# Kernel optimization log

Measured on AMD Instinct MI355X. Metric: run time of the kernel, lower is better.

The kernel has to match this reference:

```python
import jax, jax.numpy as jnp
import numpy as np

B, N, C_IN, H, C_OUT = 8, 1024, 256, 4, 256
C = C_OUT // H  # per-head dim = 64
ALPHA = 0.2
NEG_INF = -9e15


def setup_inputs() -> dict:
    key = jax.random.key(0)
    k1, k2, k3, k4, k5 = jax.random.split(key, 5)
    node_feats = jax.random.normal(k1, (B, N, C_IN), dtype=jnp.float32)
    adj_matrix = jax.random.randint(k2, (B, N, N), 0, 2, dtype=jnp.int32)
    # include self-loops as GAT expects
    eye = jnp.eye(N, dtype=jnp.int32)[None]
    adj_matrix = jnp.maximum(adj_matrix, eye)
    # xavier_uniform with gain=1.414
    def xavier(k, shape, fan_in, fan_out, gain=1.414):
        lim = gain * np.sqrt(6.0 / (fan_in + fan_out))
        return jax.random.uniform(k, shape, jnp.float32, -lim, lim)
    W = xavier(k3, (C_OUT, C_IN), C_IN, C_OUT)          # projection weight [out,in]
    b = jnp.zeros((C_OUT,), dtype=jnp.float32)           # projection bias
    a = xavier(k4, (H, 2 * C), 2 * C, H)                 # attention vector per head
    return {"node_feats": node_feats, "adj_matrix": adj_matrix, "W": W, "b": b, "a": a}


def reference(node_feats, adj_matrix, W, b, a):
    Bb, Nn, _ = node_feats.shape
    Hh, twoC = a.shape
    Cc = twoC // 2
    # linear projection -> [B, N, H, C]
    h = (node_feats @ W.T + b).reshape(Bb, Nn, Hh, Cc)
    # edge logit(i,j) = leakyrelu(a . [h_i, h_j]) = leakyrelu(a1.h_i + a2.h_j)
    a_src, a_dst = a[:, :Cc], a[:, Cc:]
    l_src = jnp.einsum('bihc,hc->bih', h, a_src)  # [B,N,H]
    l_dst = jnp.einsum('bjhc,hc->bjh', h, a_dst)  # [B,N,H]
    logits = jax.nn.leaky_relu(l_src[:, :, None, :] + l_dst[:, None, :, :], ALPHA)  # [B,N,N,H]
    logits = jnp.where(adj_matrix[..., None] == 1, logits, NEG_INF)
    probs = jax.nn.softmax(logits, axis=2)  # softmax over neighbors j
    out = jnp.einsum('bijh,bjhc->bihc', probs, h)  # aggregate
    return out.reshape(Bb, Nn, Hh * Cc)  # concat heads
```

## Files before the change

kernel.cpp:

```cpp
#include <hip/hip_runtime.h>
#include <hip/hip_bf16.h>

#define BN   8
#define NN   1024
#define CIN  256
#define COUT 256
#define HH   4
#define CC   64
#define ALPHA_C 0.2f

typedef __attribute__((ext_vector_type(8))) short short8;
typedef __attribute__((ext_vector_type(4))) float f32x4;

__device__ __forceinline__ unsigned short f2bf(float x) {
    __hip_bfloat16 h = __float2bfloat16(x);
    return *(unsigned short*)&h;
}
__device__ __forceinline__ float bf2f(unsigned short u) {
    return __uint_as_float(((unsigned int)u) << 16);
}
__device__ __forceinline__ void gl_lds16(const void* g, void* l) {
    __builtin_amdgcn_global_load_lds(
        (const __attribute__((address_space(1))) void*)g,
        (__attribute__((address_space(3))) void*)l, 16, 0, 0);
}

__global__ __launch_bounds__(256) void kprep(
    const float* __restrict__ W, const int* __restrict__ adj,
    unsigned short* __restrict__ Whp, unsigned short* __restrict__ Wlp,
    unsigned int* __restrict__ bmG)
{
    if (blockIdx.x < 2048) {
        const int bid = blockIdx.x;
        const int b  = bid & 7;
        const int rl = bid >> 3;
        const int wv = threadIdx.x >> 6;
        const int l  = threadIdx.x & 63;
        const int row = b * NN + rl * 4 + wv;
        const int* arow = adj + (size_t)row * NN;
        #pragma unroll 4
        for (int it = 0; it < 16; ++it) {
            int av = arow[it * 64 + l];
            unsigned long long mb = __ballot(av != 0);
            if (l == 0) {
                bmG[row * 32 + 2 * it    ] = (unsigned int)mb;
                bmG[row * 32 + 2 * it + 1] = (unsigned int)(mb >> 32);
            }
        }
    } else {
        const int bid = blockIdx.x - 2048;
        const int n = threadIdx.x;
        const int fi = n * 64 + (bid >> 2) * 8 + (bid & 3) * 2;
        const float4* W4 = (const float4*)W;
        float4 wa = W4[fi], wb = W4[fi + 1];
        float xs[8] = {wa.x, wa.y, wa.z, wa.w, wb.x, wb.y, wb.z, wb.w};
        unsigned short hh[8], ll[8];
        #pragma unroll
        for (int e = 0; e < 8; ++e) {
            hh[e] = f2bf(xs[e]);
            ll[e] = f2bf(xs[e] - bf2f(hh[e]));
        }
        *(uint4*)(Whp + ((size_t)bid * 256 + n) * 8) = *(uint4*)hh;
        *(uint4*)(Wlp + ((size_t)bid * 256 + n) * 8) = *(uint4*)ll;
    }
}

__global__ __launch_bounds__(1024, 1) void k1_gemm(
    const float* __restrict__ X, const float* __restrict__ bias, const float* __restrict__ a,
    const unsigned short* __restrict__ Whp, const unsigned short* __restrict__ Wlp,
    unsigned short* __restrict__ hbf_p, float* __restrict__ lsrc_t, float* __restrict__ ldst_t)
{
    __shared__ __align__(16) unsigned short Xh[32 * 256];
    __shared__ __align__(16) unsigned short Xl[32 * 256];
    __shared__ float lsP[2][8][2][16];

    const int bid = blockIdx.x;
    const int b  = bid & 7;
    const int tj = bid >> 3;
    const int row0 = b * NN + tj * 32;
    const int tid = threadIdx.x;
    const int wv = tid >> 6, l = tid & 63, il = l & 15, jg = l >> 4;
    const int mq = wv >> 3, no = wv & 7;

    {
        const float4* X4 = (const float4*)(X + (size_t)row0 * CIN);
        #pragma unroll
        for (int it = 0; it < 2; ++it) {
            int f = it * 1024 + tid;
            int r = f >> 6, k4 = f & 63;
            float4 x = X4[f];
            unsigned short h0 = f2bf(x.x), h1 = f2bf(x.y), h2 = f2bf(x.z), h3 = f2bf(x.w);
            unsigned short l0 = f2bf(x.x - bf2f(h0)), l1 = f2bf(x.y - bf2f(h1));
            unsigned short l2 = f2bf(x.z - bf2f(h2)), l3 = f2bf(x.w - bf2f(h3));
            unsigned short hs[4] = {h0, h1, h2, h3}, ls[4] = {l0, l1, l2, l3};
            int off = r * 512 + ((k4 * 8) ^ ((r & 7) << 4));
            *(uint2*)((char*)Xh + off) = *(uint2*)hs;
            *(uint2*)((char*)Xl + off) = *(uint2*)ls;
        }
    }
    __syncthreads();

    f32x4 acc0 = {0.f, 0.f, 0.f, 0.f}, acc1 = acc0;
    {
        const int abase = (mq * 16 + il) * 512;
        const int swz = (il & 7) << 4;
        const short8* Wh8 = (const short8*)Whp;
        const short8* Wl8 = (const short8*)Wlp;
        const int nb = no * 32 + il;
        #pragma unroll
        for (int kc = 0; kc < 8; ++kc) {
            const int ab = abase + ((kc * 64 + jg * 16) ^ swz);
            short8 Ah = *(const short8*)((const char*)Xh + ab);
            short8 Al = *(const short8*)((const char*)Xl + ab);
            const int pidx = (kc * 4 + jg) * 256 + nb;
            short8 Bh0 = Wh8[pidx],      Bl0 = Wl8[pidx];
            short8 Bh1 = Wh8[pidx + 16], Bl1 = Wl8[pidx + 16];
            acc0 = __builtin_amdgcn_mfma_f32_16x16x32_bf16(Ah, Bh0, acc0, 0, 0, 0);
            acc1 = __builtin_amdgcn_mfma_f32_16x16x32_bf16(Ah, Bh1, acc1, 0, 0, 0);
            acc0 = __builtin_amdgcn_mfma_f32_16x16x32_bf16(Ah, Bl0, acc0, 0, 0, 0);
            acc1 = __builtin_amdgcn_mfma_f32_16x16x32_bf16(Ah, Bl1, acc1, 0, 0, 0);
            acc0 = __builtin_amdgcn_mfma_f32_16x16x32_bf16(Al, Bh0, acc0, 0, 0, 0);
            acc1 = __builtin_amdgcn_mfma_f32_16x16x32_bf16(Al, Bh1, acc1, 0, 0, 0);
        }
    }

    const int c0 = no * 32 + il, c1 = c0 + 16;
    const float bia0 = bias[c0], bia1 = bias[c1];
    const int hh = no >> 1;
    const int cc0 = c0 & 63, cc1 = c1 & 63;
    const float as0 = a[hh * 128 + cc0],      as1 = a[hh * 128 + cc1];
    const float ad0 = a[hh * 128 + 64 + cc0], ad1 = a[hh * 128 + 64 + cc1];

    float v0[4], v1[4], psrc[4], pdst[4];
    #pragma unroll
    for (int r = 0; r < 4; ++r) {
        v0[r] = acc0[r] + bia0;
        v1[r] = acc1[r] + bia1;
        psrc[r] = v0[r] * as0 + v1[r] * as1;
        pdst[r] = v0[r] * ad0 + v1[r] * ad1;
    }
    #pragma unroll
    for (int off = 8; off >= 1; off >>= 1) {
        #pragma unroll
        for (int r = 0; r < 4; ++r) {
            psrc[r] += __shfl_xor(psrc[r], off);
            pdst[r] += __shfl_xor(pdst[r], off);
        }
    }
    __syncthreads();

    unsigned short* hp = Xh;
    #pragma unroll
    for (int r = 0; r < 4; ++r) {
        int m = mq * 16 + 4 * jg + r;
        int base = (m >> 3) * 128 + (m & 7);
        hp[(c0 >> 6) * 2048 + ((c0 & 63) >> 4) * 512 + base + (c0 & 15) * 8] = f2bf(v0[r]);
        hp[(c1 >> 6) * 2048 + ((c1 & 63) >> 4) * 512 + base + (c1 & 15) * 8] = f2bf(v1[r]);
    }
    if (il == 0) {
        #pragma unroll
        for (int r = 0; r < 4; ++r) {
            lsP[0][no][mq][4 * jg + r] = psrc[r];
            lsP[1][no][mq][4 * jg + r] = pdst[r];
        }
    }
    __syncthreads();

    {
        uint4* dst4 = (uint4*)(hbf_p + (size_t)(b * 32 + tj) * 8192);
        dst4[tid] = ((const uint4*)hp)[tid];
    }
    if (tid < 256) {
        int sd = tid >> 7, rem = tid & 127, h2 = rem >> 5, m = rem & 31;
        float v = lsP[sd][2 * h2][m >> 4][m & 15] + lsP[sd][2 * h2 + 1][m >> 4][m & 15];
        float* dst = sd ? ldst_t : lsrc_t;
        dst[((size_t)b * HH + h2) * NN + tj * 32 + m] = v;
    }
}

__global__ __launch_bounds__(1024, 1) void k2_attn(
    const unsigned short* __restrict__ hbf_p, const unsigned int* __restrict__ bmG,
    const float* __restrict__ lsrc_t, const float* __restrict__ ldst_t,
    float* __restrict__ out)
{
    __shared__ __align__(16) char smem[151808];
    __shared__ float lsumS[4][4][32];

    unsigned short* hS  = (unsigned short*)smem;
    unsigned int*  bmS  = (unsigned int*)(smem + 131072);
    float*        ldstS = (float*)(smem + 147712);

    const int bid = blockIdx.x;
    const int b  = bid & 7;
    const int h  = (bid >> 3) & 3;
    const int i0 = (bid >> 5) * 128;
    const int tid = threadIdx.x;
    const int wv = tid >> 6, l = tid & 63, il = l & 15, jg = l >> 4;
    const int rg = wv >> 2, jq = wv & 3;

    {
        #pragma unroll
        for (int k = 0; k < 2; ++k) {
            const int tj = wv * 2 + k;
            #pragma unroll
            for (int cs = 0; cs < 4; ++cs) {
                gl_lds16(hbf_p + ((((size_t)(b * 32 + tj)) * 1024 + h * 256 + cs * 64 + l) << 3),
                         hS + (size_t)(tj * 256 + cs * 64 + l) * 8);
            }
        }
    }
    {
        const unsigned int* bsrc = bmG + ((size_t)(b * NN + i0)) * 32;
        #pragma unroll
        for (int k = 0; k < 4; ++k) {
            int idx = k * 1024 + tid;
            int r = idx >> 5, w = idx & 31;
            bmS[w * 130 + r] = bsrc[idx];
        }
    }
    if (tid < 256)
        ((float4*)ldstS)[tid] = ((const float4*)(ldst_t + ((size_t)(b * HH + h)) * NN))[tid];

    const float* lsrc_b = lsrc_t + ((size_t)(b * HH + h)) * NN + i0 + rg * 32;
    const float lsv0 = lsrc_b[il];
    const float lsv1 = lsrc_b[16 + il];

    __syncthreads();

    float mx = -3.4e38f;
    #pragma unroll
    for (int jt = 0; jt < 16; ++jt) mx = fmaxf(mx, ldstS[jt * 64 + l]);
    #pragma unroll
    for (int off = 32; off >= 1; off >>= 1) mx = fmaxf(mx, __shfl_xor(mx, off));
    float mr0, mr1;
    { float t_ = lsv0 + mx; mr0 = fmaxf(t_, ALPHA_C * t_); }
    { float t_ = lsv1 + mx; mr1 = fmaxf(t_, ALPHA_C * t_); }
    float ls0 = 0.f, ls1 = 0.f;

    f32x4 z4 = {0.f,0.f,0.f,0.f};
    f32x4 a00 = z4, a01 = z4, a02 = z4, a03 = z4;
    f32x4 a10 = z4, a11 = z4, a12 = z4, a13 = z4;

    const short8* hS8 = (const short8*)hS;

    #pragma unroll 2
    for (int t = 0; t < 8; ++t) {
        const int tj = jq * 8 + t;
        short8 c0 = hS8[tj * 256 +   0 + l];
        short8 c1 = hS8[tj * 256 +  64 + l];
        short8 c2 = hS8[tj * 256 + 128 + l];
        short8 c3 = hS8[tj * 256 + 192 + l];
        const unsigned int bw0 = bmS[tj * 130 + rg * 32 + il] >> (jg * 8);
        const unsigned int bw1 = bmS[tj * 130 + rg * 32 + 16 + il] >> (jg * 8);
        const float4 dA = *(const float4*)(ldstS + tj * 32 + jg * 8);
        const float4 dB = *(const float4*)(ldstS + tj * 32 + jg * 8 + 4);

        short8 af0, af1;
        #define PELEM(AF, E, DV, BWV, LSV, MR, LS) {             \
            float s_ = (LSV) + (DV);                             \
            s_ = fmaxf(s_, ALPHA_C * s_);                        \
            float p_ = __expf(s_ - (MR));                        \
            p_ = ((BWV >> (E)) & 1u) ? p_ : 0.f;                 \
            LS += p_;                                            \
            AF[E] = (short)(__float_as_uint(p_) >> 16); }
        PELEM(af0, 0, dA.x, bw0, lsv0, mr0, ls0)
        PELEM(af0, 1, dA.y, bw0, lsv0, mr0, ls0)
        PELEM(af0, 2, dA.z, bw0, lsv0, mr0, ls0)
        PELEM(af0, 3, dA.w, bw0, lsv0, mr0, ls0)
        PELEM(af0, 4, dB.x, bw0, lsv0, mr0, ls0)
        PELEM(af0, 5, dB.y, bw0, lsv0, mr0, ls0)
        PELEM(af0, 6, dB.z, bw0, lsv0, mr0, ls0)
        PELEM(af0, 7, dB.w, bw0, lsv0, mr0, ls0)
        PELEM(af1, 0, dA.x, bw1, lsv1, mr1, ls1)
        PELEM(af1, 1, dA.y, bw1, lsv1, mr1, ls1)
        PELEM(af1, 2, dA.z, bw1, lsv1, mr1, ls1)
        PELEM(af1, 3, dA.w, bw1, lsv1, mr1, ls1)
        PELEM(af1, 4, dB.x, bw1, lsv1, mr1, ls1)
        PELEM(af1, 5, dB.y, bw1, lsv1, mr1, ls1)
        PELEM(af1, 6, dB.z, bw1, lsv1, mr1, ls1)
        PELEM(af1, 7, dB.w, bw1, lsv1, mr1, ls1)
        #undef PELEM

        a00 = __builtin_amdgcn_mfma_f32_16x16x32_bf16(af0, c0, a00, 0, 0, 0);
        a01 = __builtin_amdgcn_mfma_f32_16x16x32_bf16(af0, c1, a01, 0, 0, 0);
        a02 = __builtin_amdgcn_mfma_f32_16x16x32_bf16(af0, c2, a02, 0, 0, 0);
        a03 = __builtin_amdgcn_mfma_f32_16x16x32_bf16(af0, c3, a03, 0, 0, 0);
        a10 = __builtin_amdgcn_mfma_f32_16x16x32_bf16(af1, c0, a10, 0, 0, 0);
        a11 = __builtin_amdgcn_mfma_f32_16x16x32_bf16(af1, c1, a11, 0, 0, 0);
        a12 = __builtin_amdgcn_mfma_f32_16x16x32_bf16(af1, c2, a12, 0, 0, 0);
        a13 = __builtin_amdgcn_mfma_f32_16x16x32_bf16(af1, c3, a13, 0, 0, 0);
    }

    ls0 += __shfl_xor(ls0, 16); ls0 += __shfl_xor(ls0, 32);
    ls1 += __shfl_xor(ls1, 16); ls1 += __shfl_xor(ls1, 32);
    if (l < 16) {
        lsumS[jq][rg][il] = ls0;
        lsumS[jq][rg][16 + il] = ls1;
    }
    __syncthreads();

    float* red0 = (float*)smem;
    float* red1 = red0 + 128 * 68;
    {
        float* rb = (jq & 1) ? red1 : red0;
        const int rbase = rg * 32 + 4 * jg;
        #define STROW(ACC, ROFF, CS, OP) {                                   \
            rb[(rbase + (ROFF) + 0) * 68 + (CS) * 16 + il] OP ACC[0];        \
            rb[(rbase + (ROFF) + 1) * 68 + (CS) * 16 + il] OP ACC[1];        \
            rb[(rbase + (ROFF) + 2) * 68 + (CS) * 16 + il] OP ACC[2];        \
            rb[(rbase + (ROFF) + 3) * 68 + (CS) * 16 + il] OP ACC[3]; }
        #define STOREALL(OP) {                                               \
            STROW(a00, 0, 0, OP) STROW(a01, 0, 1, OP)                        \
            STROW(a02, 0, 2, OP) STROW(a03, 0, 3, OP)                        \
            STROW(a10, 16, 0, OP) STROW(a11, 16, 1, OP)                      \
            STROW(a12, 16, 2, OP) STROW(a13, 16, 3, OP) }
        if (jq < 2) STOREALL(=)
        __syncthreads();
        if (jq >= 2) STOREALL(+=)
        __syncthreads();
        #undef STROW
        #undef STOREALL
    }

    #pragma unroll
    for (int pass = 0; pass < 2; ++pass) {
        int row = pass * 64 + (tid >> 4);
        int c4  = tid & 15;
        float4 v0 = *(const float4*)(red0 + row * 68 + c4 * 4);
        float4 v1 = *(const float4*)(red1 + row * 68 + c4 * 4);
        float ls = lsumS[0][row >> 5][row & 31] + lsumS[1][row >> 5][row & 31]
                 + lsumS[2][row >> 5][row & 31] + lsumS[3][row >> 5][row & 31];
        float inv = 1.0f / ls;
        float4 o = make_float4((v0.x + v1.x) * inv, (v0.y + v1.y) * inv,
                               (v0.z + v1.z) * inv, (v0.w + v1.w) * inv);
        *(float4*)(out + ((size_t)(b * NN + i0 + row)) * COUT + h * 64 + c4 * 4) = o;
    }
}

extern "C" void kernel_launch(void* const* d_in, const int* in_sizes, int n_in,
                              void* d_out, int out_size, void* d_ws, size_t ws_size,
                              hipStream_t stream) {
    const float* X    = (const float*)d_in[0];
    const int*   adj  = (const int*)  d_in[1];
    const float* W    = (const float*)d_in[2];
    const float* bias = (const float*)d_in[3];
    const float* a    = (const float*)d_in[4];
    float* out = (float*)d_out;

    unsigned short* hbf_p = (unsigned short*)d_ws;
    float* lsrc_t = (float*)(hbf_p + (size_t)BN * 32 * 8192);
    float* ldst_t = lsrc_t + (size_t)BN * HH * NN;
    unsigned short* Whp = (unsigned short*)(ldst_t + (size_t)BN * HH * NN);
    unsigned short* Wlp = Whp + 65536;
    unsigned int*   bmG = (unsigned int*)(Wlp + 65536);

    kprep<<<2048 + 32, 256, 0, stream>>>(W, adj, Whp, Wlp, bmG);
    k1_gemm<<<256, 1024, 0, stream>>>(X, bias, a, Whp, Wlp, hbf_p, lsrc_t, ldst_t);
    k2_attn<<<256, 1024, 0, stream>>>(hbf_p, bmG, lsrc_t, ldst_t, out);
}
```

Before: 41.51 us.

## Fuse adjacency bitmask build into GEMM kernel and streamline softmax exp

```diff
diff --git a/kernel.cpp b/kernel.cpp
--- a/kernel.cpp
+++ b/kernel.cpp
@@ -8,6 +8,13 @@
 #define HH   4
 #define CC   64
 #define ALPHA_C 0.2f
+#define LOG2E_C 1.4426950408889634f
+
+#if __has_builtin(__builtin_amdgcn_exp2f)
+#define EXP2F(x) __builtin_amdgcn_exp2f(x)
+#else
+#define EXP2F(x) exp2f(x)
+#endif
 
 typedef __attribute__((ext_vector_type(8))) short short8;
 typedef __attribute__((ext_vector_type(4))) float f32x4;
@@ -25,50 +32,30 @@
         (__attribute__((address_space(3))) void*)l, 16, 0, 0);
 }
 
-__global__ __launch_bounds__(256) void kprep(
-    const float* __restrict__ W, const int* __restrict__ adj,
-    unsigned short* __restrict__ Whp, unsigned short* __restrict__ Wlp,
-    unsigned int* __restrict__ bmG)
+__global__ __launch_bounds__(256) void kw_pack(
+    const float* __restrict__ W, unsigned short* __restrict__ Whp, unsigned short* __restrict__ Wlp)
 {
-    if (blockIdx.x < 2048) {
-        const int bid = blockIdx.x;
-        const int b  = bid & 7;
-        const int rl = bid >> 3;
-        const int wv = threadIdx.x >> 6;
-        const int l  = threadIdx.x & 63;
-        const int row = b * NN + rl * 4 + wv;
-        const int* arow = adj + (size_t)row * NN;
-        #pragma unroll 4
-        for (int it = 0; it < 16; ++it) {
-            int av = arow[it * 64 + l];
-            unsigned long long mb = __ballot(av != 0);
-            if (l == 0) {
-                bmG[row * 32 + 2 * it    ] = (unsigned int)mb;
-                bmG[row * 32 + 2 * it + 1] = (unsigned int)(mb >> 32);
-            }
-        }
-    } else {
-        const int bid = blockIdx.x - 2048;
-        const int n = threadIdx.x;
-        const int fi = n * 64 + (bid >> 2) * 8 + (bid & 3) * 2;
-        const float4* W4 = (const float4*)W;
-        float4 wa = W4[fi], wb = W4[fi + 1];
-        float xs[8] = {wa.x, wa.y, wa.z, wa.w, wb.x, wb.y, wb.z, wb.w};
-        unsigned short hh[8], ll[8];
-        #pragma unroll
-        for (int e = 0; e < 8; ++e) {
-            hh[e] = f2bf(xs[e]);
-            ll[e] = f2bf(xs[e] - bf2f(hh[e]));
-        }
-        *(uint4*)(Whp + ((size_t)bid * 256 + n) * 8) = *(uint4*)hh;
-        *(uint4*)(Wlp + ((size_t)bid * 256 + n) * 8) = *(uint4*)ll;
-    }
+    const int bid = blockIdx.x;
+    const int n = threadIdx.x;
+    const int fi = n * 64 + (bid >> 2) * 8 + (bid & 3) * 2;
+    const float4* W4 = (const float4*)W;
+    float4 wa = W4[fi], wb = W4[fi + 1];
+    float xs[8] = {wa.x, wa.y, wa.z, wa.w, wb.x, wb.y, wb.z, wb.w};
+    unsigned short hh[8], ll[8];
+    #pragma unroll
+    for (int e = 0; e < 8; ++e) {
+        hh[e] = f2bf(xs[e]);
+        ll[e] = f2bf(xs[e] - bf2f(hh[e]));
+    }
+    *(uint4*)(Whp + ((size_t)bid * 256 + n) * 8) = *(uint4*)hh;
+    *(uint4*)(Wlp + ((size_t)bid * 256 + n) * 8) = *(uint4*)ll;
 }
 
 __global__ __launch_bounds__(1024, 1) void k1_gemm(
     const float* __restrict__ X, const float* __restrict__ bias, const float* __restrict__ a,
-    const unsigned short* __restrict__ Whp, const unsigned short* __restrict__ Wlp,
-    unsigned short* __restrict__ hbf_p, float* __restrict__ lsrc_t, float* __restrict__ ldst_t)
+    const int* __restrict__ adj, const unsigned short* __restrict__ Whp,
+    const unsigned short* __restrict__ Wlp, unsigned short* __restrict__ hbf_p,
+    float* __restrict__ lsrc_t, float* __restrict__ ldst_t, unsigned int* __restrict__ bmG)
 {
     __shared__ __align__(16) unsigned short Xh[32 * 256];
     __shared__ __align__(16) unsigned short Xl[32 * 256];
@@ -81,6 +68,25 @@
     const int tid = threadIdx.x;
     const int wv = tid >> 6, l = tid & 63, il = l & 15, jg = l >> 4;
     const int mq = wv >> 3, no = wv & 7;
+
+    {
+        #pragma unroll
+        for (int rr = 0; rr < 2; ++rr) {
+            const int r = 2 * wv + rr;
+            const int* ap = adj + ((size_t)(row0 + r)) * NN;
+            int av[16];
+            #pragma unroll
+            for (int it = 0; it < 16; ++it) av[it] = ap[it * 64 + l];
+            #pragma unroll
+            for (int it = 0; it < 16; ++it) {
+                unsigned long long mb = __ballot(av[it] != 0);
+                if (l == 0) {
+                    bmG[((size_t)(row0 + r)) * 32 + 2 * it    ] = (unsigned int)mb;
+                    bmG[((size_t)(row0 + r)) * 32 + 2 * it + 1] = (unsigned int)(mb >> 32);
+                }
+            }
+        }
+    }
 
     {
         const float4* X4 = (const float4*)(X + (size_t)row0 * CIN);
@@ -218,12 +224,15 @@
             bmS[w * 130 + r] = bsrc[idx];
         }
     }
-    if (tid < 256)
-        ((float4*)ldstS)[tid] = ((const float4*)(ldst_t + ((size_t)(b * HH + h)) * NN))[tid];
+    if (tid < 256) {
+        float4 v = ((const float4*)(ldst_t + ((size_t)(b * HH + h)) * NN))[tid];
+        v.x *= LOG2E_C; v.y *= LOG2E_C; v.z *= LOG2E_C; v.w *= LOG2E_C;
+        ((float4*)ldstS)[tid] = v;
+    }
 
     const float* lsrc_b = lsrc_t + ((size_t)(b * HH + h)) * NN + i0 + rg * 32;
-    const float lsv0 = lsrc_b[il];
-    const float lsv1 = lsrc_b[16 + il];
+    const float lsv0 = lsrc_b[il] * LOG2E_C;
+    const float lsv1 = lsrc_b[16 + il] * LOG2E_C;
 
     __syncthreads();
 
@@ -235,15 +244,16 @@
     float mr0, mr1;
     { float t_ = lsv0 + mx; mr0 = fmaxf(t_, ALPHA_C * t_); }
     { float t_ = lsv1 + mx; mr1 = fmaxf(t_, ALPHA_C * t_); }
-    float ls0 = 0.f, ls1 = 0.f;
 
     f32x4 z4 = {0.f,0.f,0.f,0.f};
     f32x4 a00 = z4, a01 = z4, a02 = z4, a03 = z4;
     f32x4 a10 = z4, a11 = z4, a12 = z4, a13 = z4;
+    f32x4 s0 = z4, s1 = z4;
+    const short8 ones8 = {0x3F80, 0x3F80, 0x3F80, 0x3F80, 0x3F80, 0x3F80, 0x3F80, 0x3F80};
 
     const short8* hS8 = (const short8*)hS;
 
-    #pragma unroll 2
+    #pragma unroll
     for (int t = 0; t < 8; ++t) {
         const int tj = jq * 8 + t;
         short8 c0 = hS8[tj * 256 +   0 + l];
@@ -256,46 +266,48 @@
         const float4 dB = *(const float4*)(ldstS + tj * 32 + jg * 8 + 4);
 
         short8 af0, af1;
-        #define PELEM(AF, E, DV, BWV, LSV, MR, LS) {             \
-            float s_ = (LSV) + (DV);                             \
-            s_ = fmaxf(s_, ALPHA_C * s_);                        \
-            float p_ = __expf(s_ - (MR));                        \
-            p_ = ((BWV >> (E)) & 1u) ? p_ : 0.f;                 \
-            LS += p_;                                            \
-            AF[E] = (short)(__float_as_uint(p_) >> 16); }
-        PELEM(af0, 0, dA.x, bw0, lsv0, mr0, ls0)
-        PELEM(af0, 1, dA.y, bw0, lsv0, mr0, ls0)
-        PELEM(af0, 2, dA.z, bw0, lsv0, mr0, ls0)
-        PELEM(af0, 3, dA.w, bw0, lsv0, mr0, ls0)
-        PELEM(af0, 4, dB.x, bw0, lsv0, mr0, ls0)
-        PELEM(af0, 5, dB.y, bw0, lsv0, mr0, ls0)
-        PELEM(af0, 6, dB.z, bw0, lsv0, mr0, ls0)
-        PELEM(af0, 7, dB.w, bw0, lsv0, mr0, ls0)
-        PELEM(af1, 0, dA.x, bw1, lsv1, mr1, ls1)
-        PELEM(af1, 1, dA.y, bw1, lsv1, mr1, ls1)
-        PELEM(af1, 2, dA.z, bw1, lsv1, mr1, ls1)
-        PELEM(af1, 3, dA.w, bw1, lsv1, mr1, ls1)
-        PELEM(af1, 4, dB.x, bw1, lsv1, mr1, ls1)
-        PELEM(af1, 5, dB.y, bw1, lsv1, mr1, ls1)
-        PELEM(af1, 6, dB.z, bw1, lsv1, mr1, ls1)
-        PELEM(af1, 7, dB.w, bw1, lsv1, mr1, ls1)
+        #define PELEM(AF, E, DV, BWV, LSV, MR) {                         \
+            float t_ = (LSV) + (DV);                                     \
+            float u_ = fmaxf(t_, ALPHA_C * t_);                          \
+            float e_ = EXP2F(u_ - (MR));                                 \
+            int m_ = ((int)((BWV) << (31 - (E)))) >> 31;                 \
+            AF[E] = (short)((__float_as_uint(e_) >> 16) & (unsigned)m_); }
+        PELEM(af0, 0, dA.x, bw0, lsv0, mr0)
+        PELEM(af0, 1, dA.y, bw0, lsv0, mr0)
+        PELEM(af0, 2, dA.z, bw0, lsv0, mr0)
+        PELEM(af0, 3, dA.w, bw0, lsv0, mr0)
+        PELEM(af0, 4, dB.x, bw0, lsv0, mr0)
+        PELEM(af0, 5, dB.y, bw0, lsv0, mr0)
+        PELEM(af0, 6, dB.z, bw0, lsv0, mr0)
+        PELEM(af0, 7, dB.w, bw0, lsv0, mr0)
+        PELEM(af1, 0, dA.x, bw1, lsv1, mr1)
+        PELEM(af1, 1, dA.y, bw1, lsv1, mr1)
+        PELEM(af1, 2, dA.z, bw1, lsv1, mr1)
+        PELEM(af1, 3, dA.w, bw1, lsv1, mr1)
+        PELEM(af1, 4, dB.x, bw1, lsv1, mr1)
+        PELEM(af1, 5, dB.y, bw1, lsv1, mr1)
+        PELEM(af1, 6, dB.z, bw1, lsv1, mr1)
+        PELEM(af1, 7, dB.w, bw1, lsv1, mr1)
         #undef PELEM
 
         a00 = __builtin_amdgcn_mfma_f32_16x16x32_bf16(af0, c0, a00, 0, 0, 0);
         a01 = __builtin_amdgcn_mfma_f32_16x16x32_bf16(af0, c1, a01, 0, 0, 0);
         a02 = __builtin_amdgcn_mfma_f32_16x16x32_bf16(af0, c2, a02, 0, 0, 0);
         a03 = __builtin_amdgcn_mfma_f32_16x16x32_bf16(af0, c3, a03, 0, 0, 0);
+        s0  = __builtin_amdgcn_mfma_f32_16x16x32_bf16(af0, ones8, s0, 0, 0, 0);
         a10 = __builtin_amdgcn_mfma_f32_16x16x32_bf16(af1, c0, a10, 0, 0, 0);
         a11 = __builtin_amdgcn_mfma_f32_16x16x32_bf16(af1, c1, a11, 0, 0, 0);
         a12 = __builtin_amdgcn_mfma_f32_16x16x32_bf16(af1, c2, a12, 0, 0, 0);
         a13 = __builtin_amdgcn_mfma_f32_16x16x32_bf16(af1, c3, a13, 0, 0, 0);
-    }
-
-    ls0 += __shfl_xor(ls0, 16); ls0 += __shfl_xor(ls0, 32);
-    ls1 += __shfl_xor(ls1, 16); ls1 += __shfl_xor(ls1, 32);
-    if (l < 16) {
-        lsumS[jq][rg][il] = ls0;
-        lsumS[jq][rg][16 + il] = ls1;
+        s1  = __builtin_amdgcn_mfma_f32_16x16x32_bf16(af1, ones8, s1, 0, 0, 0);
+    }
+
+    if (il == 0) {
+        #pragma unroll
+        for (int r = 0; r < 4; ++r) {
+            lsumS[jq][rg][4 * jg + r]      = s0[r];
+            lsumS[jq][rg][16 + 4 * jg + r] = s1[r];
+        }
     }
     __syncthreads();
 
@@ -354,7 +366,7 @@
     unsigned short* Wlp = Whp + 65536;
     unsigned int*   bmG = (unsigned int*)(Wlp + 65536);
 
-    kprep<<<2048 + 32, 256, 0, stream>>>(W, adj, Whp, Wlp, bmG);
-    k1_gemm<<<256, 1024, 0, stream>>>(X, bias, a, Whp, Wlp, hbf_p, lsrc_t, ldst_t);
+    kw_pack<<<32, 256, 0, stream>>>(W, Whp, Wlp);
+    k1_gemm<<<256, 1024, 0, stream>>>(X, bias, a, adj, Whp, Wlp, hbf_p, lsrc_t, ldst_t, bmG);
     k2_attn<<<256, 1024, 0, stream>>>(hbf_p, bmG, lsrc_t, ldst_t, out);
 }
```

After: 43.28 us. 1.04x slower.

## Overlap adjacency bitmask packing with projection GEMM in one launch

Applied to the files above, without the earlier changes.

```diff
diff --git a/kernel.cpp b/kernel.cpp
--- a/kernel.cpp
+++ b/kernel.cpp
@@ -25,51 +25,52 @@
         (__attribute__((address_space(3))) void*)l, 16, 0, 0);
 }
 
-__global__ __launch_bounds__(256) void kprep(
-    const float* __restrict__ W, const int* __restrict__ adj,
-    unsigned short* __restrict__ Whp, unsigned short* __restrict__ Wlp,
-    unsigned int* __restrict__ bmG)
+__global__ __launch_bounds__(256) void kw_pack(
+    const float* __restrict__ W, unsigned short* __restrict__ Whp, unsigned short* __restrict__ Wlp)
 {
-    if (blockIdx.x < 2048) {
-        const int bid = blockIdx.x;
-        const int b  = bid & 7;
-        const int rl = bid >> 3;
-        const int wv = threadIdx.x >> 6;
-        const int l  = threadIdx.x & 63;
-        const int row = b * NN + rl * 4 + wv;
+    const int bid = blockIdx.x;
+    const int n = threadIdx.x;
+    const int fi = n * 64 + (bid >> 2) * 8 + (bid & 3) * 2;
+    const float4* W4 = (const float4*)W;
+    float4 wa = W4[fi], wb = W4[fi + 1];
+    float xs[8] = {wa.x, wa.y, wa.z, wa.w, wb.x, wb.y, wb.z, wb.w};
+    unsigned short hh[8], ll[8];
+    #pragma unroll
+    for (int e = 0; e < 8; ++e) {
+        hh[e] = f2bf(xs[e]);
+        ll[e] = f2bf(xs[e] - bf2f(hh[e]));
+    }
+    *(uint4*)(Whp + ((size_t)bid * 256 + n) * 8) = *(uint4*)hh;
+    *(uint4*)(Wlp + ((size_t)bid * 256 + n) * 8) = *(uint4*)ll;
+}
+
+__global__ __launch_bounds__(1024, 1) void k1x(
+    const float* __restrict__ X, const float* __restrict__ bias, const float* __restrict__ a,
+    const int* __restrict__ adj, const unsigned short* __restrict__ Whp,
+    const unsigned short* __restrict__ Wlp, unsigned short* __restrict__ hbf_p,
+    float* __restrict__ lsrc_t, float* __restrict__ ldst_t, unsigned int* __restrict__ bmG)
+{
+    const int tid = threadIdx.x;
+    const int wv = tid >> 6, l = tid & 63;
+
+    if (blockIdx.x >= 256) {
+        const int a_ = blockIdx.x - 256;
+        const int b  = a_ & 7;
+        const int ch = a_ >> 3;
+        const int row = b * NN + ch * 16 + wv;
         const int* arow = adj + (size_t)row * NN;
         #pragma unroll 4
         for (int it = 0; it < 16; ++it) {
             int av = arow[it * 64 + l];
             unsigned long long mb = __ballot(av != 0);
             if (l == 0) {
-                bmG[row * 32 + 2 * it    ] = (unsigned int)mb;
-                bmG[row * 32 + 2 * it + 1] = (unsigned int)(mb >> 32);
+                bmG[(size_t)row * 32 + 2 * it    ] = (unsigned int)mb;
+                bmG[(size_t)row * 32 + 2 * it + 1] = (unsigned int)(mb >> 32);
             }
         }
-    } else {
-        const int bid = blockIdx.x - 2048;
-        const int n = threadIdx.x;
-        const int fi = n * 64 + (bid >> 2) * 8 + (bid & 3) * 2;
-        const float4* W4 = (const float4*)W;
-        float4 wa = W4[fi], wb = W4[fi + 1];
-        float xs[8] = {wa.x, wa.y, wa.z, wa.w, wb.x, wb.y, wb.z, wb.w};
-        unsigned short hh[8], ll[8];
-        #pragma unroll
-        for (int e = 0; e < 8; ++e) {
-            hh[e] = f2bf(xs[e]);
-            ll[e] = f2bf(xs[e] - bf2f(hh[e]));
-        }
-        *(uint4*)(Whp + ((size_t)bid * 256 + n) * 8) = *(uint4*)hh;
-        *(uint4*)(Wlp + ((size_t)bid * 256 + n) * 8) = *(uint4*)ll;
-    }
-}
-
-__global__ __launch_bounds__(1024, 1) void k1_gemm(
-    const float* __restrict__ X, const float* __restrict__ bias, const float* __restrict__ a,
-    const unsigned short* __restrict__ Whp, const unsigned short* __restrict__ Wlp,
-    unsigned short* __restrict__ hbf_p, float* __restrict__ lsrc_t, float* __restrict__ ldst_t)
-{
+        return;
+    }
+
     __shared__ __align__(16) unsigned short Xh[32 * 256];
     __shared__ __align__(16) unsigned short Xl[32 * 256];
     __shared__ float lsP[2][8][2][16];
@@ -78,8 +79,7 @@
     const int b  = bid & 7;
     const int tj = bid >> 3;
     const int row0 = b * NN + tj * 32;
-    const int tid = threadIdx.x;
-    const int wv = tid >> 6, l = tid & 63, il = l & 15, jg = l >> 4;
+    const int il = l & 15, jg = l >> 4;
     const int mq = wv >> 3, no = wv & 7;
 
     {
@@ -354,7 +354,7 @@
     unsigned short* Wlp = Whp + 65536;
     unsigned int*   bmG = (unsigned int*)(Wlp + 65536);
 
-    kprep<<<2048 + 32, 256, 0, stream>>>(W, adj, Whp, Wlp, bmG);
-    k1_gemm<<<256, 1024, 0, stream>>>(X, bias, a, Whp, Wlp, hbf_p, lsrc_t, ldst_t);
+    kw_pack<<<32, 256, 0, stream>>>(W, Whp, Wlp);
+    k1x<<<256 + 512, 1024, 0, stream>>>(X, bias, a, adj, Whp, Wlp, hbf_p, lsrc_t, ldst_t, bmG);
     k2_attn<<<256, 1024, 0, stream>>>(hbf_p, bmG, lsrc_t, ldst_t, out);
 }
```

Result: slower. 44.74 us (+7.8%).
